# Kernel tuning notes

Measured on AMD Instinct MI355X. Metric: run time of the kernel, lower is better.

The kernel has to match this reference:

```python
import jax, jax.numpy as jnp
import numpy as np
from jax import lax

B, T_ENC, E = 32, 256, 512
A_RNN, D_RNN, P = 1024, 1024, 256
N_MEL, T_DEC = 80, 800
A_DIM, N_FILT, K = 128, 32, 31
PAD = (K - 1) // 2


def setup_inputs() -> dict:
    key = jax.random.key(0)
    ks = jax.random.split(key, 20)
    rn = lambda k, s, sc=0.02: jax.random.normal(k, s, dtype=jnp.float32) * sc
    return {
        "encoder_outputs": jax.random.normal(ks[0], (B, T_ENC, E), dtype=jnp.float32),
        "decoder_inputs": jax.random.normal(ks[1], (B, N_MEL, T_DEC), dtype=jnp.float32),
        "input_lengths": jax.random.randint(ks[2], (B,), 128, T_ENC + 1),
        "prenet_w1": rn(ks[3], (P, N_MEL)),
        "prenet_w2": rn(ks[4], (P, P)),
        "attn_rnn_Wih": rn(ks[5], (4 * A_RNN, P + E)),
        "attn_rnn_Whh": rn(ks[6], (4 * A_RNN, A_RNN)),
        "attn_rnn_bih": jnp.zeros((4 * A_RNN,), jnp.float32),
        "attn_rnn_bhh": jnp.zeros((4 * A_RNN,), jnp.float32),
        "query_W": rn(ks[7], (A_RNN, A_DIM)),
        "memory_W": rn(ks[8], (E, A_DIM)),
        "v_w": rn(ks[9], (A_DIM,)),
        "loc_conv_W": rn(ks[10], (N_FILT, 2, K)),
        "loc_lin_W": rn(ks[11], (N_FILT, A_DIM)),
        "dec_rnn_Wih": rn(ks[12], (4 * D_RNN, A_RNN + E)),
        "dec_rnn_Whh": rn(ks[13], (4 * D_RNN, D_RNN)),
        "dec_rnn_bih": jnp.zeros((4 * D_RNN,), jnp.float32),
        "dec_rnn_bhh": jnp.zeros((4 * D_RNN,), jnp.float32),
        "proj_W": rn(ks[14], (D_RNN + E, N_MEL)),
        "proj_b": jnp.zeros((N_MEL,), jnp.float32),
        "gate_W": rn(ks[15], (D_RNN + E, 1)),
        "gate_b": jnp.zeros((1,), jnp.float32),
    }


def _lstm_cell(xin, h0, c0, Wih, Whh, bih, bhh):
    # PyTorch LSTMCell gate order: i, f, g, o
    g = xin @ Wih.T + bih + h0 @ Whh.T + bhh
    i, f, gg, o = jnp.split(g, 4, axis=-1)
    c = jax.nn.sigmoid(f) * c0 + jax.nn.sigmoid(i) * jnp.tanh(gg)
    return jax.nn.sigmoid(o) * jnp.tanh(c), c


def _forward(encoder_outputs, decoder_inputs, prenet_w1, prenet_w2,
             attn_rnn_Wih, attn_rnn_Whh, attn_rnn_bih, attn_rnn_bhh,
             query_W, memory_W, v_w, loc_conv_W, loc_lin_W,
             dec_rnn_Wih, dec_rnn_Whh, dec_rnn_bih, dec_rnn_bhh,
             proj_W, proj_b, gate_W, gate_b, input_lengths):
    b, t_enc, e = encoder_outputs.shape
    n_mel = decoder_inputs.shape[1]
    dt = encoder_outputs.dtype

    # parse_decoder_inputs + go frame; keep the T_dec frames actually consumed
    x = jnp.transpose(decoder_inputs, (2, 0, 1))               # [T_dec, B, n_mel]
    go = jnp.zeros((1, b, n_mel), dt)
    x = jnp.concatenate([go, x], 0)[:-1]                       # [T_dec, B, n_mel]

    # Prenet: relu->dropout(p=0.5, always on) x2 (deterministic keys)
    k1, k2 = jax.random.split(jax.random.key(42))
    h = jax.nn.relu(jnp.einsum('tbm,pm->tbp', x, prenet_w1))
    h = h * jax.random.bernoulli(k1, 0.5, h.shape) * 2.0
    h = jax.nn.relu(jnp.einsum('tbp,qp->tbq', h, prenet_w2))
    pre = h * jax.random.bernoulli(k2, 0.5, h.shape) * 2.0     # [T_dec, B, P]

    valid = jnp.arange(t_enc)[None, :] < input_lengths[:, None]  # [B, T_enc]
    pmem = jnp.einsum('bte,ea->bta', encoder_outputs, memory_W)  # processed memory

    def step(carry, xstep):
        ah, ac, dh, dc, ctx, aw, awc = carry
        ah, ac = _lstm_cell(jnp.concatenate([xstep, ctx], -1), ah, ac,
                            attn_rnn_Wih, attn_rnn_Whh, attn_rnn_bih, attn_rnn_bhh)
        # location-sensitive attention (LSA)
        loc = jnp.stack([aw, awc], 1)                           # [B, 2, T_enc]
        lf = lax.conv_general_dilated(loc, loc_conv_W, (1,), [(PAD, PAD)],
                                      dimension_numbers=('NCH', 'OIH', 'NCH'))
        lf = jnp.einsum('bft,fa->bta', lf, loc_lin_W)           # [B, T_enc, A_DIM]
        q = ah @ query_W                                        # [B, A_DIM]
        energies = jnp.tanh(q[:, None, :] + lf + pmem) @ v_w    # [B, T_enc]
        energies = jnp.where(valid, energies, jnp.asarray(-1e9, dt))
        aw = jax.nn.softmax(energies, axis=-1)
        awc = awc + aw
        ctx = jnp.einsum('bt,bte->be', aw, encoder_outputs)
        dh, dc = _lstm_cell(jnp.concatenate([ah, ctx], -1), dh, dc,
                            dec_rnn_Wih, dec_rnn_Whh, dec_rnn_bih, dec_rnn_bhh)
        hc = jnp.concatenate([dh, ctx], -1)
        mel = hc @ proj_W + proj_b                              # [B, n_mel]
        gate = (hc @ gate_W + gate_b)[:, 0]                     # [B]
        return (ah, ac, dh, dc, ctx, aw, awc), (mel, gate, aw)

    z = lambda d: jnp.zeros((b, d), dt)
    carry0 = (z(A_RNN), z(A_RNN), z(D_RNN), z(D_RNN), z(e),
              jnp.zeros((b, t_enc), dt), jnp.zeros((b, t_enc), dt))
    _, (mels, gates, aligns) = lax.scan(step, carry0, pre)

    mel_outputs = jnp.transpose(mels, (1, 2, 0))                # [B, n_mel, T_dec]
    gate_outputs = gates.T                                      # [B, T_dec]
    alignments = jnp.transpose(aligns, (1, 0, 2))               # [B, T_dec, T_enc]
    return mel_outputs, gate_outputs, alignments


def reference(encoder_outputs, decoder_inputs, input_lengths, prenet_w1, prenet_w2,
              attn_rnn_Wih, attn_rnn_Whh, attn_rnn_bih, attn_rnn_bhh,
              query_W, memory_W, v_w, loc_conv_W, loc_lin_W,
              dec_rnn_Wih, dec_rnn_Whh, dec_rnn_bih, dec_rnn_bhh,
              proj_W, proj_b, gate_W, gate_b):
    return _forward(encoder_outputs, decoder_inputs, prenet_w1, prenet_w2,
                    attn_rnn_Wih, attn_rnn_Whh, attn_rnn_bih, attn_rnn_bhh,
                    query_W, memory_W, v_w, loc_conv_W, loc_lin_W,
                    dec_rnn_Wih, dec_rnn_Whh, dec_rnn_bih, dec_rnn_bhh,
                    proj_W, proj_b, gate_W, gate_b, input_lengths)
```

## Files before the change

### kernel.cpp

```cpp
#include <hip/hip_runtime.h>
#include <hip/hip_cooperative_groups.h>
#include <cstdint>
#include <cstddef>

constexpr int TDEC   = 800;
constexpr int KCONV  = 31;

constexpr int AH_OFF   = 0;
constexpr int AC_OFF   = 65536;
constexpr int DH_OFF   = 98304;
constexpr int DC_OFF   = 163840;
constexpr int CTX_OFF  = 196608;
constexpr int AW_OFF   = 229376;
constexpr int AWC_OFF  = 237568;
constexpr int BAR_OFF  = 245760;
constexpr int STATE_FLOATS = 253952;
constexpr int PRE_OFF  = 253952;
constexpr int PMEM_OFF = 6807552;
constexpr int W1T_OFF  = 7856128;
constexpr int W2T_OFF  = 7876608;
constexpr int LINT_OFF = 7942144;

typedef __attribute__((ext_vector_type(4))) float f32x4;
typedef __attribute__((ext_vector_type(4))) unsigned int u32x4;

__device__ __forceinline__ void coh_load4(const float* p, f32x4& v) {
  asm volatile("global_load_dwordx4 %0, %1, off sc0 sc1" : "=v"(v) : "v"(p));
}
__device__ __forceinline__ void coh_load1(const float* p, float& v) {
  asm volatile("global_load_dword %0, %1, off sc0 sc1" : "=v"(v) : "v"(p));
}
__device__ __forceinline__ void coh_store1(float* p, float v) {
  asm volatile("global_store_dword %0, %1, off sc0 sc1" :: "v"(p), "v"(v) : "memory");
}
__device__ __forceinline__ void coh_wait() {
  asm volatile("s_waitcnt vmcnt(0)" ::: "memory");
  __builtin_amdgcn_sched_barrier(0);
}

__device__ __forceinline__ void gbar(uint32_t* slots, uint32_t val) {
  asm volatile("s_waitcnt vmcnt(0)" ::: "memory");
  __syncthreads();
  if (threadIdx.x == 0) {
    uint32_t* p = slots + blockIdx.x;
    asm volatile("global_store_dword %0, %1, off sc0 sc1" :: "v"(p), "v"(val) : "memory");
  }
  if (threadIdx.x < 64) {
    const uint32_t* sp = slots + threadIdx.x * 4;
    while (true) {
      u32x4 v4;
      asm volatile("global_load_dwordx4 %0, %1, off sc0 sc1" : "=v"(v4) : "v"(sp) : "memory");
      asm volatile("s_waitcnt vmcnt(0)" ::: "memory");
      if (v4.x >= val && v4.y >= val && v4.z >= val && v4.w >= val) break;
      __builtin_amdgcn_s_sleep(2);
    }
  }
  __syncthreads();
}

__host__ __device__ inline void tf2x32(uint32_t k0, uint32_t k1, uint32_t& x0, uint32_t& x1) {
  const uint32_t ks2 = k0 ^ k1 ^ 0x1BD11BDAu;
  uint32_t y0 = x0 + k0, y1 = x1 + k1;
#define TFR(r) { y0 += y1; y1 = (y1 << (r)) | (y1 >> (32 - (r))); y1 ^= y0; }
  TFR(13) TFR(15) TFR(26) TFR(6)   y0 += k1;  y1 += ks2 + 1u;
  TFR(17) TFR(29) TFR(16) TFR(24)  y0 += ks2; y1 += k0 + 2u;
  TFR(13) TFR(15) TFR(26) TFR(6)   y0 += k0;  y1 += k1 + 3u;
  TFR(17) TFR(29) TFR(16) TFR(24)  y0 += k1;  y1 += ks2 + 4u;
  TFR(13) TFR(15) TFR(26) TFR(6)   y0 += ks2; y1 += k0 + 5u;
#undef TFR
  x0 = y0; x1 = y1;
}

__device__ inline bool tf_keep(uint32_t ka, uint32_t kb, uint32_t i) {
  uint32_t x0 = 0u, x1 = i;
  tf2x32(ka, kb, x0, x1);
  return (((x0 ^ x1) >> 31) == 0u);
}

__device__ inline float sigm(float x) { return 1.f / (1.f + expf(-x)); }

__global__ __launch_bounds__(256) void transpose_k(const float* __restrict__ src,
                                                   float* __restrict__ dst, int R, int C) {
  int i = blockIdx.x * 256 + threadIdx.x;
  if (i < R * C) { int r = i / C, c = i % C; dst[c * R + r] = src[i]; }
}

__global__ __launch_bounds__(256) void prenet1_kernel(const float* __restrict__ decin,
                                                      const float* __restrict__ w1T,
                                                      float* __restrict__ pre,
                                                      uint32_t ka, uint32_t kb) {
  __shared__ float xs[32][81];
  const int t = blockIdx.x, tid = threadIdx.x;
  for (int f = tid; f < 32 * 80; f += 256) {
    int b = f / 80, m = f % 80;
    xs[b][m] = (t == 0) ? 0.f : decin[b * 64000 + m * 800 + (t - 1)];
  }
  __syncthreads();
  const int p = tid;
  float acc[32];
#pragma unroll
  for (int r = 0; r < 32; ++r) acc[r] = 0.f;
  for (int m = 0; m < 80; ++m) {
    float wv = w1T[m * 256 + p];
#pragma unroll
    for (int r = 0; r < 32; ++r) acc[r] += xs[r][m] * wv;
  }
  float* rowbase = pre + (size_t)t * 32 * 256;
#pragma unroll
  for (int r = 0; r < 32; ++r) {
    float v = fmaxf(acc[r], 0.f);
    uint32_t i = (uint32_t)((t * 32 + r) * 256 + p);
    rowbase[r * 256 + p] = tf_keep(ka, kb, i) ? v * 2.f : 0.f;
  }
}

__global__ __launch_bounds__(256) void prenet2_kernel(const float* __restrict__ w2T,
                                                      float* __restrict__ pre,
                                                      uint32_t ka, uint32_t kb) {
  __shared__ float hs[32][257];
  const int t = blockIdx.x, tid = threadIdx.x;
  float* rowbase = pre + (size_t)t * 32 * 256;
  for (int f = tid; f < 32 * 256; f += 256) {
    int b = f >> 8, k = f & 255;
    hs[b][k] = rowbase[b * 256 + k];
  }
  __syncthreads();
  const int p = tid;
  float acc[32];
#pragma unroll
  for (int r = 0; r < 32; ++r) acc[r] = 0.f;
  for (int k = 0; k < 256; ++k) {
    float wv = w2T[k * 256 + p];
#pragma unroll
    for (int r = 0; r < 32; ++r) acc[r] += hs[r][k] * wv;
  }
#pragma unroll
  for (int r = 0; r < 32; ++r) {
    float v = fmaxf(acc[r], 0.f);
    uint32_t i = (uint32_t)((t * 32 + r) * 256 + p);
    rowbase[r * 256 + p] = tf_keep(ka, kb, i) ? v * 2.f : 0.f;
  }
}

__global__ __launch_bounds__(128) void pmem_kernel(const float* __restrict__ enc,
                                                   const float* __restrict__ memW,
                                                   float* __restrict__ pmem) {
  __shared__ float es[8][513];
  const int b = blockIdx.x >> 5, tg = blockIdx.x & 31, t0 = tg * 8;
  const int tid = threadIdx.x;
  for (int f = tid; f < 8 * 512; f += 128) {
    int rr = f >> 9, e = f & 511;
    es[rr][e] = enc[(size_t)(b * 256 + t0 + rr) * 512 + e];
  }
  __syncthreads();
  float acc[8];
#pragma unroll
  for (int r = 0; r < 8; ++r) acc[r] = 0.f;
  const int a = tid;
  for (int e = 0; e < 512; ++e) {
    float wv = memW[e * 128 + a];
#pragma unroll
    for (int r = 0; r < 8; ++r) acc[r] += es[r][e] * wv;
  }
#pragma unroll
  for (int r = 0; r < 8; ++r) pmem[(size_t)(b * 256 + t0 + r) * 128 + a] = acc[r];
}

struct ScanParams {
  const float* enc; const int* lens;
  const float* aWih; const float* aWhh; const float* abih; const float* abhh;
  const float* qW;   const float* vw;   const float* locW; const float* linT;
  const float* dWih; const float* dWhh; const float* dbih; const float* dbhh;
  const float* pW;   const float* pb;   const float* gW;   const float* gb;
  float* ah; float* ac; float* dh; float* dc; float* ctx; float* aw; float* awc;
  uint32_t* bar;
  const float* pre; const float* pmem;
  float* mel_out; float* gate_out; float* align_out;
};

constexpr int SMEM_F = 12480;

struct XW { const float* x; int ldx; const float* w; int ldw; int coh; };

__device__ __forceinline__ void stage_load(const XW& ch, f32x4* sreg, int tid) {
#pragma unroll
  for (int u = 0; u < 2; ++u) {
    int f4 = tid * 2 + u;
    int bs = f4 >> 6;
    int kk = (f4 & 63) * 4;
    const float* p = ch.x + (size_t)bs * ch.ldx + kk;
    if (ch.coh) coh_load4(p, sreg[u]);
    else        sreg[u] = *(const f32x4*)p;
  }
}
__device__ __forceinline__ void stage_store(const f32x4* sreg, float* dst, int tid) {
#pragma unroll
  for (int u = 0; u < 2; ++u) {
    int f4 = tid * 2 + u;
    int bs = f4 >> 6;
    int kk = (f4 & 63) * 4;
    *(f32x4*)(dst + bs * 256 + kk) = sreg[u];
  }
}

template <typename F>
__device__ __forceinline__ void lstm_core(int blk, int tid, int nc, F getc,
                                          const float* bih, const float* bhh,
                                          float* hout, float* cst, float* smem) {
  const int lane = tid & 63;
  const int bg = (tid >> 6) & 3;
  const int jg = tid >> 8;
  const int b0 = bg * 8;
  const int hb = blk * 4;
  float* xs = smem;
  float* gate_s = smem + 8192;

  float acc[4][8];
#pragma unroll
  for (int rr = 0; rr < 4; ++rr) {
    float bv = (lane == 0) ? (bih[jg * 1024 + hb + rr] + bhh[jg * 1024 + hb + rr]) : 0.f;
#pragma unroll
    for (int bb = 0; bb < 8; ++bb) acc[rr][bb] = bv;
  }

  f32x4 sreg[2];
  {
    XW c0 = getc(0);
    stage_load(c0, sreg, tid);
    coh_wait();
    stage_store(sreg, xs, tid);
  }
  float4 wc[4];
  {
    XW c0 = getc(0);
#pragma unroll
    for (int rr = 0; rr < 4; ++rr)
      wc[rr] = *(const float4*)(c0.w + (size_t)(jg * 1024 + hb + rr) * c0.ldw + lane * 4);
  }
  __syncthreads();

  for (int c = 0; c < nc; ++c) {
    float4 wn[4];
    const bool more = (c + 1 < nc);
    if (more) {
      XW cn = getc(c + 1);
      stage_load(cn, sreg, tid);
#pragma unroll
      for (int rr = 0; rr < 4; ++rr)
        wn[rr] = *(const float4*)(cn.w + (size_t)(jg * 1024 + hb + rr) * cn.ldw + lane * 4);
    }
#pragma unroll
    for (int bb = 0; bb < 8; ++bb) {
      float4 x4 = *(const float4*)(xs + (b0 + bb) * 256 + lane * 4);
#pragma unroll
      for (int rr = 0; rr < 4; ++rr) {
        acc[rr][bb] = fmaf(wc[rr].x, x4.x, acc[rr][bb]);
        acc[rr][bb] = fmaf(wc[rr].y, x4.y, acc[rr][bb]);
        acc[rr][bb] = fmaf(wc[rr].z, x4.z, acc[rr][bb]);
        acc[rr][bb] = fmaf(wc[rr].w, x4.w, acc[rr][bb]);
      }
    }
    __syncthreads();
    if (more) {
      coh_wait();
      stage_store(sreg, xs, tid);
#pragma unroll
      for (int rr = 0; rr < 4; ++rr) wc[rr] = wn[rr];
      __syncthreads();
    }
  }

  float v[32];
#pragma unroll
  for (int rr = 0; rr < 4; ++rr)
#pragma unroll
    for (int bb = 0; bb < 8; ++bb) v[rr * 8 + bb] = acc[rr][bb];
#pragma unroll
  for (int s = 0; s < 5; ++s) {
    const int d = 32 >> s;
    const int half = 32 >> (s + 1);
    const bool up = (lane & d) != 0;
#pragma unroll
    for (int i = 0; i < 16; ++i) {
      if (i < half) {
        float send = up ? v[i] : v[i + half];
        float got = __shfl_xor(send, d);
        v[i] = (up ? v[i + half] : v[i]) + got;
      }
    }
  }
  v[0] += __shfl_xor(v[0], 1);
  if ((lane & 1) == 0) {
    int p = (lane >> 1) & 31;
    int rr = p >> 3, bb = p & 7;
    gate_s[(jg * 4 + rr) * 33 + (b0 + bb)] = v[0];
  }
  __syncthreads();
  if (tid < 128) {
    int hl = tid >> 5, b = tid & 31;
    float gi = gate_s[(0 + hl) * 33 + b];
    float gf = gate_s[(4 + hl) * 33 + b];
    float gg = gate_s[(8 + hl) * 33 + b];
    float go = gate_s[(12 + hl) * 33 + b];
    int idx = b * 1024 + hb + hl;
    float c0v = cst[idx];
    float cn = sigm(gf) * c0v + sigm(gi) * tanhf(gg);
    cst[idx] = cn;
    coh_store1(hout + idx, sigm(go) * tanhf(cn));
  }
  __syncthreads();
}

__device__ void stage_attn(int b, int tid, int t, const ScanParams& P,
                           const float* ah_cur, float* ctx_out, float* smem) {
  float* part = smem;
  float* sLoc = smem + 1024;
  float* q_s  = smem + 1600;
  float* vw_s = smem + 1728;
  float* red  = smem + 1856;
  float* aw_s = smem + 1888;
  float* cpart= smem + 2144;
  float* ah_l = smem + 3168;
  float* lf_s = smem + 4192;

  float ahv;
  coh_load1(ah_cur + b * 1024 + tid, ahv);
  if (tid < 572) {
    int c = tid / 286, i = tid % 286;
    int src = i - 15;
    float vv = 0.f;
    if (src >= 0 && src < 256) vv = (c == 0 ? P.aw : P.awc)[b * 256 + src];
    sLoc[c * 286 + i] = vv;
  } else if (tid < 700) {
    vw_s[tid - 572] = P.vw[tid - 572];
  }
  coh_wait();
  ah_l[tid] = ahv;
  __syncthreads();
  {
    const int js = tid >> 7, a = tid & 127;
    const float* ahb = ah_l + js * 128;
    const float* qp = P.qW + (size_t)(js * 128) * 128 + a;
    float p0 = 0.f, p1 = 0.f, p2 = 0.f, p3 = 0.f;
    for (int j = 0; j < 128; j += 4) {
      p0 += ahb[j] * qp[(size_t)j * 128];
      p1 += ahb[j + 1] * qp[(size_t)(j + 1) * 128];
      p2 += ahb[j + 2] * qp[(size_t)(j + 2) * 128];
      p3 += ahb[j + 3] * qp[(size_t)(j + 3) * 128];
    }
    part[tid] = (p0 + p1) + (p2 + p3);
  }
  __syncthreads();
  if (tid < 128) {
    float q = 0.f;
#pragma unroll
    for (int js = 0; js < 8; ++js) q += part[js * 128 + tid];
    q_s[tid] = q;
  }
  {
    const int f = tid >> 5, tg = tid & 31;
    float accL[8];
#pragma unroll
    for (int i = 0; i < 8; ++i) accL[i] = 0.f;
    const float* wf = P.locW + f * 62;
#pragma unroll
    for (int c = 0; c < 2; ++c)
#pragma unroll
      for (int k = 0; k < KCONV; ++k) {
        float wv = wf[c * 31 + k];
        const float* sl = sLoc + c * 286 + tg * 8 + k;
#pragma unroll
        for (int i = 0; i < 8; ++i) accL[i] += sl[i] * wv;
      }
#pragma unroll
    for (int i = 0; i < 8; ++i) lf_s[f * 258 + tg * 8 + i] = accL[i];
  }
  __syncthreads();
  {
    const int tt = tid >> 2, aq = tid & 3;
    float lfv[32];
#pragma unroll
    for (int f = 0; f < 32; ++f) lfv[f] = lf_s[f * 258 + tt];
    const float* pm = P.pmem + (size_t)(b * 256 + tt) * 128;
    float ep = 0.f;
#pragma unroll 4
    for (int ai = 0; ai < 32; ++ai) {
      int a = aq * 32 + ai;
      const float4* lt = (const float4*)(P.linT + a * 32);
      float lfa = 0.f;
#pragma unroll
      for (int u = 0; u < 8; ++u) {
        float4 l4 = lt[u];
        lfa += l4.x * lfv[u * 4] + l4.y * lfv[u * 4 + 1] + l4.z * lfv[u * 4 + 2] + l4.w * lfv[u * 4 + 3];
      }
      float val = tanhf(q_s[a] + lfa + pm[a]);
      ep += val * vw_s[a];
    }
    part[tid] = ep;
  }
  __syncthreads();
  const int len_b = P.lens[b];
  if (tid < 256) {
    float e = part[tid * 4] + part[tid * 4 + 1] + part[tid * 4 + 2] + part[tid * 4 + 3];
    e = (tid < len_b) ? e : -1e9f;
    aw_s[tid] = e;
  }
  __syncthreads();
  if (tid < 64) {
    float m0 = fmaxf(fmaxf(aw_s[tid], aw_s[64 + tid]), fmaxf(aw_s[128 + tid], aw_s[192 + tid]));
#pragma unroll
    for (int m = 32; m >= 1; m >>= 1) m0 = fmaxf(m0, __shfl_xor(m0, m));
    if (tid == 0) red[0] = m0;
  }
  __syncthreads();
  const float mx = red[0];
  if (tid < 256) part[tid] = expf(aw_s[tid] - mx);
  __syncthreads();
  if (tid < 64) {
    float s0 = part[tid] + part[64 + tid] + part[128 + tid] + part[192 + tid];
#pragma unroll
    for (int m = 32; m >= 1; m >>= 1) s0 += __shfl_xor(s0, m);
    if (tid == 0) red[1] = s0;
  }
  __syncthreads();
  const float inv = 1.f / red[1];
  if (tid < 256) {
    float awv = part[tid] * inv;
    aw_s[tid] = awv;
    P.aw[b * 256 + tid] = awv;
    P.awc[b * 256 + tid] += awv;
    P.align_out[(size_t)b * 204800 + (size_t)t * 256 + tid] = awv;
  }
  __syncthreads();
  {
    const int ee = tid & 511, hf = tid >> 9;
    const float* encb = P.enc + (size_t)b * 131072 + (size_t)hf * 128 * 512 + ee;
    float a0 = 0.f, a1 = 0.f, a2 = 0.f, a3 = 0.f;
    for (int tt = 0; tt < 128; tt += 4) {
      a0 += aw_s[hf * 128 + tt] * encb[(size_t)tt * 512];
      a1 += aw_s[hf * 128 + tt + 1] * encb[(size_t)(tt + 1) * 512];
      a2 += aw_s[hf * 128 + tt + 2] * encb[(size_t)(tt + 2) * 512];
      a3 += aw_s[hf * 128 + tt + 3] * encb[(size_t)(tt + 3) * 512];
    }
    cpart[hf * 512 + ee] = (a0 + a1) + (a2 + a3);
  }
  __syncthreads();
  if (tid < 512) coh_store1(ctx_out + b * 512 + tid, cpart[tid] + cpart[512 + tid]);
}

__device__ void stage_proj(int b, int tid, int tp, const ScanParams& P,
                           const float* dh_prev, const float* ctx_prev, float* smem) {
  float* hc    = smem;
  float* partm = smem + 1536;
  float* partg = smem + 2016;
  for (int i = tid; i < 1536; i += 1024) {
    float v;
    const float* p = (i < 1024) ? (dh_prev + b * 1024 + i) : (ctx_prev + b * 512 + (i - 1024));
    coh_load1(p, v);
    coh_wait();
    hc[i] = v;
  }
  __syncthreads();
  if (tid < 480) {
    int ks = tid / 80, m = tid % 80;
    const float* pWk = P.pW + (size_t)(ks * 256) * 80 + m;
    const float* hck = hc + ks * 256;
    float a0 = 0.f, a1 = 0.f, a2 = 0.f, a3 = 0.f;
    for (int k = 0; k < 256; k += 4) {
      a0 += hck[k] * pWk[(size_t)k * 80];
      a1 += hck[k + 1] * pWk[(size_t)(k + 1) * 80];
      a2 += hck[k + 2] * pWk[(size_t)(k + 2) * 80];
      a3 += hck[k + 3] * pWk[(size_t)(k + 3) * 80];
    }
    partm[ks * 80 + m] = (a0 + a1) + (a2 + a3);
  } else if (tid < 512) {
    int s = tid - 480;
    float acc = 0.f;
    for (int k = s * 48; k < s * 48 + 48; ++k) acc += hc[k] * P.gW[k];
    partg[s] = acc;
  }
  __syncthreads();
  if (tid < 80) {
    float acc = P.pb[tid];
#pragma unroll
    for (int s = 0; s < 6; ++s) acc += partm[s * 80 + tid];
    P.mel_out[b * 64000 + tid * 800 + tp] = acc;
  }
  if (tid == 511) {
    float acc = P.gb[0];
#pragma unroll
    for (int s = 0; s < 32; ++s) acc += partg[s];
    P.gate_out[b * 800 + tp] = acc;
  }
  __syncthreads();
}

__global__ void __launch_bounds__(1024, 4) scan_kernel(ScanParams P) {
  const int blk = blockIdx.x, tid = threadIdx.x;
  __shared__ float smem[SMEM_F];
  uint32_t* slots = P.bar;
  uint32_t bk = 0;

  for (int i = 0; i <= TDEC; ++i) {
    const int pi = i & 1, pim1 = pi ^ 1;
    if (i < TDEC) {
      const float* pre_t = P.pre + (size_t)i * 8192;
      const float* ctx_r = P.ctx + pim1 * 16384;
      const float* ah_r  = P.ah + pim1 * 32768;
      const ScanParams& Q = P;
      auto getc1 = [&](int c) -> XW {
        XW r;
        if (c == 0)      { r.x = pre_t;                 r.ldx = 256;  r.w = Q.aWih;                        r.ldw = 768;  r.coh = 0; }
        else if (c <= 2) { r.x = ctx_r + (c - 1) * 256; r.ldx = 512;  r.w = Q.aWih + 256 + (c - 1) * 256;  r.ldw = 768;  r.coh = 1; }
        else             { r.x = ah_r + (c - 3) * 256;  r.ldx = 1024; r.w = Q.aWhh + (c - 3) * 256;        r.ldw = 1024; r.coh = 1; }
        return r;
      };
      lstm_core(blk, tid, 7, getc1, P.abih, P.abhh, P.ah + pi * 32768, P.ac, smem);
    }
    if (i >= 1) {
      const float* ah_r  = P.ah + pim1 * 32768;
      const float* ctx_r = P.ctx + pim1 * 16384;
      const float* dh_r  = P.dh + pi * 32768;
      const ScanParams& Q = P;
      auto getc2 = [&](int c) -> XW {
        XW r;
        if (c <= 3)      { r.x = ah_r + c * 256;        r.ldx = 1024; r.w = Q.dWih + c * 256;              r.ldw = 1536; r.coh = 1; }
        else if (c <= 5) { r.x = ctx_r + (c - 4) * 256; r.ldx = 512;  r.w = Q.dWih + 1024 + (c - 4) * 256; r.ldw = 1536; r.coh = 1; }
        else             { r.x = dh_r + (c - 6) * 256;  r.ldx = 1024; r.w = Q.dWhh + (c - 6) * 256;        r.ldw = 1024; r.coh = 1; }
        return r;
      };
      lstm_core(blk, tid, 10, getc2, P.dbih, P.dbhh, P.dh + pim1 * 32768, P.dc, smem);
    }
    gbar(slots, ++bk);
    if (blk < 32) {
      if (i < TDEC) stage_attn(blk, tid, i, P, P.ah + pi * 32768, P.ctx + pi * 16384, smem);
    } else if (blk < 64) {
      if (i >= 1) stage_proj(blk - 32, tid, i - 1, P, P.dh + pim1 * 32768, P.ctx + pim1 * 16384, smem);
    }
    gbar(slots, ++bk);
  }
}

extern "C" void kernel_launch(void* const* d_in, const int* in_sizes, int n_in,
                              void* d_out, int out_size, void* d_ws, size_t ws_size,
                              hipStream_t stream) {
  (void)in_sizes; (void)n_in; (void)out_size; (void)ws_size;
  const float* enc   = (const float*)d_in[0];
  const float* decin = (const float*)d_in[1];
  const int*   lens  = (const int*)d_in[2];
  const float* w1    = (const float*)d_in[3];
  const float* w2    = (const float*)d_in[4];
  const float* aWih  = (const float*)d_in[5];
  const float* aWhh  = (const float*)d_in[6];
  const float* abih  = (const float*)d_in[7];
  const float* abhh  = (const float*)d_in[8];
  const float* qW    = (const float*)d_in[9];
  const float* memW  = (const float*)d_in[10];
  const float* vw    = (const float*)d_in[11];
  const float* locW  = (const float*)d_in[12];
  const float* linW  = (const float*)d_in[13];
  const float* dWih  = (const float*)d_in[14];
  const float* dWhh  = (const float*)d_in[15];
  const float* dbih  = (const float*)d_in[16];
  const float* dbhh  = (const float*)d_in[17];
  const float* pW    = (const float*)d_in[18];
  const float* pb    = (const float*)d_in[19];
  const float* gW    = (const float*)d_in[20];
  const float* gb    = (const float*)d_in[21];

  float* ws  = (float*)d_ws;
  float* out = (float*)d_out;

  hipMemsetAsync(ws, 0, (size_t)STATE_FLOATS * sizeof(float), stream);

  uint32_t k1a, k1b, k2a, k2b;
  { uint32_t a = 0u, b = 0u; tf2x32(0u, 42u, a, b); k1a = a; k1b = b; }
  { uint32_t a = 0u, b = 1u; tf2x32(0u, 42u, a, b); k2a = a; k2b = b; }

  transpose_k<<<dim3((256 * 80 + 255) / 256), dim3(256), 0, stream>>>(w1, ws + W1T_OFF, 256, 80);
  transpose_k<<<dim3((256 * 256 + 255) / 256), dim3(256), 0, stream>>>(w2, ws + W2T_OFF, 256, 256);
  transpose_k<<<dim3((32 * 128 + 255) / 256), dim3(256), 0, stream>>>(linW, ws + LINT_OFF, 32, 128);
  prenet1_kernel<<<dim3(800), dim3(256), 0, stream>>>(decin, ws + W1T_OFF, ws + PRE_OFF, k1a, k1b);
  prenet2_kernel<<<dim3(800), dim3(256), 0, stream>>>(ws + W2T_OFF, ws + PRE_OFF, k2a, k2b);
  pmem_kernel<<<dim3(1024), dim3(128), 0, stream>>>(enc, memW, ws + PMEM_OFF);

  ScanParams prm;
  prm.enc = enc; prm.lens = lens;
  prm.aWih = aWih; prm.aWhh = aWhh; prm.abih = abih; prm.abhh = abhh;
  prm.qW = qW; prm.vw = vw; prm.locW = locW; prm.linT = ws + LINT_OFF;
  prm.dWih = dWih; prm.dWhh = dWhh; prm.dbih = dbih; prm.dbhh = dbhh;
  prm.pW = pW; prm.pb = pb; prm.gW = gW; prm.gb = gb;
  prm.ah = ws + AH_OFF; prm.ac = ws + AC_OFF;
  prm.dh = ws + DH_OFF; prm.dc = ws + DC_OFF;
  prm.ctx = ws + CTX_OFF; prm.aw = ws + AW_OFF; prm.awc = ws + AWC_OFF;
  prm.bar = (uint32_t*)(ws + BAR_OFF);
  prm.pre = ws + PRE_OFF; prm.pmem = ws + PMEM_OFF;
  prm.mel_out = out; prm.gate_out = out + 2048000; prm.align_out = out + 2073600;

  void* kargs[] = { (void*)&prm };
  hipLaunchCooperativeKernel(scan_kernel, dim3(256), dim3(1024), kargs, 0, stream);
}
```

Before: 382.4 ms.

## Keep LSTM weight high halves resident in LDS and stream low halves from a prepacked blob

Each of the 256 persistent blocks now splits its slice of the attention and decoder LSTM weights into high and low 16-bit halves. The high halves are kept resident in LDS for the whole 800-step scan, and the low halves are read from a prepacked, lane-ordered global blob built by a new pre-kernel. The full fp32 weight is rebuilt in registers, so each step no longer re-reads all fp32 weights from global memory or L2. The location-conv/energy stage is also reorganised into two 128-position halves with a shuffle reduction so it fits the smaller scratch area. This costs about 160KB of dynamic LDS per block, which limits occupancy, and adds a one-time packing pass at kernel start.

Measured after the change: 391.7 ms. 1.02x slower.

```diff
diff --git a/kernel.cpp b/kernel.cpp
--- a/kernel.cpp
+++ b/kernel.cpp
@@ -2,9 +2,9 @@
 #include <hip/hip_cooperative_groups.h>
 #include <cstdint>
 #include <cstddef>
+#include <cstring>
 
 constexpr int TDEC   = 800;
-constexpr int KCONV  = 31;
 
 constexpr int AH_OFF   = 0;
 constexpr int AC_OFF   = 65536;
@@ -20,6 +20,13 @@
 constexpr int W1T_OFF  = 7856128;
 constexpr int W2T_OFF  = 7876608;
 constexpr int LINT_OFF = 7942144;
+constexpr int BLOB_OFF = 7946240;
+constexpr int WCHUNKS_A = 14;
+constexpr int WCHUNKS_D = 20;
+constexpr int WBLK_DW  = 34816;
+
+constexpr int SCRATCH_F     = 5376;
+constexpr int SMEM_BYTES    = 139264 + SCRATCH_F * 4;
 
 typedef __attribute__((ext_vector_type(4))) float f32x4;
 typedef __attribute__((ext_vector_type(4))) unsigned int u32x4;
@@ -79,6 +86,20 @@
 
 __device__ inline float sigm(float x) { return 1.f / (1.f + expf(-x)); }
 
+__device__ __forceinline__ const float* wsrc(int c, int j, int kk,
+                                             const float* aWih, const float* aWhh,
+                                             const float* dWih, const float* dWhh) {
+  if (c < WCHUNKS_A) {
+    int k = c * 128 + kk;
+    return (k < 768) ? (aWih + (size_t)j * 768 + k)
+                     : (aWhh + (size_t)j * 1024 + (k - 768));
+  } else {
+    int k = (c - WCHUNKS_A) * 128 + kk;
+    return (k < 1536) ? (dWih + (size_t)j * 1536 + k)
+                      : (dWhh + (size_t)j * 1024 + (k - 1536));
+  }
+}
+
 __global__ __launch_bounds__(256) void transpose_k(const float* __restrict__ src,
                                                    float* __restrict__ dst, int R, int C) {
   int i = blockIdx.x * 256 + threadIdx.x;
@@ -166,6 +187,29 @@
   for (int r = 0; r < 8; ++r) pmem[(size_t)(b * 256 + t0 + r) * 128 + a] = acc[r];
 }
 
+__global__ __launch_bounds__(1024) void mklo_kernel(const float* __restrict__ aWih,
+                                                    const float* __restrict__ aWhh,
+                                                    const float* __restrict__ dWih,
+                                                    const float* __restrict__ dWhh,
+                                                    uint32_t* __restrict__ blob) {
+  __shared__ float tmp[2048];
+  const int blk = blockIdx.x, tid = threadIdx.x;
+  uint32_t* bdst = blob + (size_t)blk * WBLK_DW;
+  for (int c = 0; c < WCHUNKS_A + WCHUNKS_D; ++c) {
+    const int row16 = tid >> 6;
+    const int kk = (tid & 63) * 2;
+    const int j = (row16 >> 2) * 1024 + blk * 4 + (row16 & 3);
+    float2 wv = *(const float2*)wsrc(c, j, kk, aWih, aWhh, dWih, dWhh);
+    *(float2*)(tmp + row16 * 128 + kk) = wv;
+    __syncthreads();
+    const int rr = tid & 3, jgq = (tid >> 2) & 3, l = tid >> 4;
+    uint32_t b0 = __float_as_uint(tmp[(jgq * 4 + rr) * 128 + l * 2]) & 0xffffu;
+    uint32_t b1 = __float_as_uint(tmp[(jgq * 4 + rr) * 128 + l * 2 + 1]) & 0xffffu;
+    bdst[c * 1024 + (l * 4 + jgq) * 4 + rr] = b0 | (b1 << 16);
+    __syncthreads();
+  }
+}
+
 struct ScanParams {
   const float* enc; const int* lens;
   const float* aWih; const float* aWhh; const float* abih; const float* abhh;
@@ -173,47 +217,25 @@
   const float* dWih; const float* dWhh; const float* dbih; const float* dbhh;
   const float* pW;   const float* pb;   const float* gW;   const float* gb;
   float* ah; float* ac; float* dh; float* dc; float* ctx; float* aw; float* awc;
-  uint32_t* bar;
+  uint32_t* bar; const uint32_t* wlo;
   const float* pre; const float* pmem;
   float* mel_out; float* gate_out; float* align_out;
 };
 
-constexpr int SMEM_F = 12480;
-
-struct XW { const float* x; int ldx; const float* w; int ldw; int coh; };
-
-__device__ __forceinline__ void stage_load(const XW& ch, f32x4* sreg, int tid) {
-#pragma unroll
-  for (int u = 0; u < 2; ++u) {
-    int f4 = tid * 2 + u;
-    int bs = f4 >> 6;
-    int kk = (f4 & 63) * 4;
-    const float* p = ch.x + (size_t)bs * ch.ldx + kk;
-    if (ch.coh) coh_load4(p, sreg[u]);
-    else        sreg[u] = *(const f32x4*)p;
-  }
-}
-__device__ __forceinline__ void stage_store(const f32x4* sreg, float* dst, int tid) {
-#pragma unroll
-  for (int u = 0; u < 2; ++u) {
-    int f4 = tid * 2 + u;
-    int bs = f4 >> 6;
-    int kk = (f4 & 63) * 4;
-    *(f32x4*)(dst + bs * 256 + kk) = sreg[u];
-  }
-}
+struct XW { const float* x; int ldx; int coh; };
 
 template <typename F>
-__device__ __forceinline__ void lstm_core(int blk, int tid, int nc, F getc,
-                                          const float* bih, const float* bhh,
-                                          float* hout, float* cst, float* smem) {
+__device__ __forceinline__ void lstm_lds(int blk, int tid, int nc, F getx,
+                                         const uint32_t* wch0, const uint32_t* lch0,
+                                         const float* bih, const float* bhh,
+                                         float* hout, float* cst,
+                                         float* xs, float* gate_s) {
   const int lane = tid & 63;
   const int bg = (tid >> 6) & 3;
   const int jg = tid >> 8;
   const int b0 = bg * 8;
-  const int hb = blk * 4;
-  float* xs = smem;
-  float* gate_s = smem + 8192;
+  const int hb = blk << 2;
+  const int woff = (lane * 4 + jg) << 2;
 
   float acc[4][8];
 #pragma unroll
@@ -223,49 +245,49 @@
     for (int bb = 0; bb < 8; ++bb) acc[rr][bb] = bv;
   }
 
-  f32x4 sreg[2];
+  const int sb = tid >> 5;
+  const int skq = (tid & 31) * 4;
+  f32x4 sreg;
+  u32x4 lcur, lnxt;
   {
-    XW c0 = getc(0);
-    stage_load(c0, sreg, tid);
-    coh_wait();
-    stage_store(sreg, xs, tid);
-  }
-  float4 wc[4];
-  {
-    XW c0 = getc(0);
-#pragma unroll
-    for (int rr = 0; rr < 4; ++rr)
-      wc[rr] = *(const float4*)(c0.w + (size_t)(jg * 1024 + hb + rr) * c0.ldw + lane * 4);
+    XW x0 = getx(0);
+    const float* p = x0.x + (size_t)sb * x0.ldx + skq;
+    lcur = *(const u32x4*)(lch0 + woff);
+    if (x0.coh) { coh_load4(p, sreg); coh_wait(); }
+    else        sreg = *(const f32x4*)p;
+    *(f32x4*)(xs + sb * 132 + skq) = sreg;
   }
   __syncthreads();
 
   for (int c = 0; c < nc; ++c) {
-    float4 wn[4];
     const bool more = (c + 1 < nc);
     if (more) {
-      XW cn = getc(c + 1);
-      stage_load(cn, sreg, tid);
+      XW xn = getx(c + 1);
+      const float* p = xn.x + (size_t)sb * xn.ldx + skq;
+      lnxt = *(const u32x4*)(lch0 + (c + 1) * 1024 + woff);
+      if (xn.coh) coh_load4(p, sreg);
+      else        sreg = *(const f32x4*)p;
+    }
+    u32x4 wv = *(const u32x4*)(wch0 + c * 1024 + woff);
+    float we[4], wo[4];
+#pragma unroll
+    for (int rr = 0; rr < 4; ++rr) {
+      uint32_t h = wv[rr], l = lcur[rr];
+      we[rr] = __uint_as_float((h << 16) | (l & 0xffffu));
+      wo[rr] = __uint_as_float((h & 0xffff0000u) | (l >> 16));
+    }
+#pragma unroll
+    for (int bb = 0; bb < 8; ++bb) {
+      float2 x2 = *(const float2*)(xs + (b0 + bb) * 132 + lane * 2);
 #pragma unroll
       for (int rr = 0; rr < 4; ++rr)
-        wn[rr] = *(const float4*)(cn.w + (size_t)(jg * 1024 + hb + rr) * cn.ldw + lane * 4);
-    }
-#pragma unroll
-    for (int bb = 0; bb < 8; ++bb) {
-      float4 x4 = *(const float4*)(xs + (b0 + bb) * 256 + lane * 4);
-#pragma unroll
-      for (int rr = 0; rr < 4; ++rr) {
-        acc[rr][bb] = fmaf(wc[rr].x, x4.x, acc[rr][bb]);
-        acc[rr][bb] = fmaf(wc[rr].y, x4.y, acc[rr][bb]);
-        acc[rr][bb] = fmaf(wc[rr].z, x4.z, acc[rr][bb]);
-        acc[rr][bb] = fmaf(wc[rr].w, x4.w, acc[rr][bb]);
-      }
+        acc[rr][bb] = fmaf(wo[rr], x2.y, fmaf(we[rr], x2.x, acc[rr][bb]));
     }
     __syncthreads();
     if (more) {
       coh_wait();
-      stage_store(sreg, xs, tid);
-#pragma unroll
-      for (int rr = 0; rr < 4; ++rr) wc[rr] = wn[rr];
+      *(f32x4*)(xs + sb * 132 + skq) = sreg;
+      lcur = lnxt;
       __syncthreads();
     }
   }
@@ -312,16 +334,16 @@
 }
 
 __device__ void stage_attn(int b, int tid, int t, const ScanParams& P,
-                           const float* ah_cur, float* ctx_out, float* smem) {
-  float* part = smem;
-  float* sLoc = smem + 1024;
-  float* q_s  = smem + 1600;
-  float* vw_s = smem + 1728;
-  float* red  = smem + 1856;
-  float* aw_s = smem + 1888;
-  float* cpart= smem + 2144;
-  float* ah_l = smem + 3168;
-  float* lf_s = smem + 4192;
+                           const float* ah_cur, float* ctx_out, float* S) {
+  float* ah_l = S;
+  float* part = S + 1024;
+  float* lf   = S;
+  float* sLoc = S + 4224;
+  float* q_s  = S + 4800;
+  float* vw_s = S + 4928;
+  float* red  = S + 5056;
+  float* aw_s = S + 5064;
+  float* cpart= S + 1024;
 
   float ahv;
   coh_load1(ah_cur + b * 1024 + tid, ahv);
@@ -357,55 +379,54 @@
     for (int js = 0; js < 8; ++js) q += part[js * 128 + tid];
     q_s[tid] = q;
   }
-  {
-    const int f = tid >> 5, tg = tid & 31;
-    float accL[8];
-#pragma unroll
-    for (int i = 0; i < 8; ++i) accL[i] = 0.f;
-    const float* wf = P.locW + f * 62;
-#pragma unroll
-    for (int c = 0; c < 2; ++c)
-#pragma unroll
-      for (int k = 0; k < KCONV; ++k) {
-        float wv = wf[c * 31 + k];
-        const float* sl = sLoc + c * 286 + tg * 8 + k;
-#pragma unroll
-        for (int i = 0; i < 8; ++i) accL[i] += sl[i] * wv;
+  __syncthreads();
+  const int len_b = P.lens[b];
+#pragma unroll 1
+  for (int h = 0; h < 2; ++h) {
+    const int tt0 = h << 7;
+    {
+      const int f = tid >> 5, seg = tid & 31;
+      float a0 = 0.f, a1 = 0.f, a2 = 0.f, a3 = 0.f;
+      const float* wf = P.locW + f * 62;
+#pragma unroll
+      for (int c2 = 0; c2 < 2; ++c2)
+#pragma unroll
+        for (int k = 0; k < 31; ++k) {
+          float wv = wf[c2 * 31 + k];
+          const float* sl = sLoc + c2 * 286 + tt0 + seg * 4 + k;
+          a0 = fmaf(sl[0], wv, a0); a1 = fmaf(sl[1], wv, a1);
+          a2 = fmaf(sl[2], wv, a2); a3 = fmaf(sl[3], wv, a3);
+        }
+      lf[(seg * 4 + 0) * 33 + f] = a0; lf[(seg * 4 + 1) * 33 + f] = a1;
+      lf[(seg * 4 + 2) * 33 + f] = a2; lf[(seg * 4 + 3) * 33 + f] = a3;
+    }
+    __syncthreads();
+    {
+      const int ttl = tid >> 3, aq = tid & 7;
+      const int tt = tt0 + ttl;
+      const float* pm = P.pmem + (size_t)(b * 256 + tt) * 128;
+      const float* lfr = lf + ttl * 33;
+      float lfv[32];
+#pragma unroll
+      for (int f = 0; f < 32; ++f) lfv[f] = lfr[f];
+      float ep = 0.f;
+#pragma unroll 2
+      for (int ai = 0; ai < 16; ++ai) {
+        int a = aq * 16 + ai;
+        const float4* lt = (const float4*)(P.linT + a * 32);
+        float lfa = 0.f;
+#pragma unroll
+        for (int u = 0; u < 8; ++u) {
+          float4 l4 = lt[u];
+          lfa += l4.x * lfv[u * 4] + l4.y * lfv[u * 4 + 1] + l4.z * lfv[u * 4 + 2] + l4.w * lfv[u * 4 + 3];
+        }
+        ep += vw_s[a] * tanhf(q_s[a] + lfa + pm[a]);
       }
-#pragma unroll
-    for (int i = 0; i < 8; ++i) lf_s[f * 258 + tg * 8 + i] = accL[i];
-  }
-  __syncthreads();
-  {
-    const int tt = tid >> 2, aq = tid & 3;
-    float lfv[32];
-#pragma unroll
-    for (int f = 0; f < 32; ++f) lfv[f] = lf_s[f * 258 + tt];
-    const float* pm = P.pmem + (size_t)(b * 256 + tt) * 128;
-    float ep = 0.f;
-#pragma unroll 4
-    for (int ai = 0; ai < 32; ++ai) {
-      int a = aq * 32 + ai;
-      const float4* lt = (const float4*)(P.linT + a * 32);
-      float lfa = 0.f;
-#pragma unroll
-      for (int u = 0; u < 8; ++u) {
-        float4 l4 = lt[u];
-        lfa += l4.x * lfv[u * 4] + l4.y * lfv[u * 4 + 1] + l4.z * lfv[u * 4 + 2] + l4.w * lfv[u * 4 + 3];
-      }
-      float val = tanhf(q_s[a] + lfa + pm[a]);
-      ep += val * vw_s[a];
-    }
-    part[tid] = ep;
-  }
-  __syncthreads();
-  const int len_b = P.lens[b];
-  if (tid < 256) {
-    float e = part[tid * 4] + part[tid * 4 + 1] + part[tid * 4 + 2] + part[tid * 4 + 3];
-    e = (tid < len_b) ? e : -1e9f;
-    aw_s[tid] = e;
-  }
-  __syncthreads();
+      ep += __shfl_xor(ep, 1); ep += __shfl_xor(ep, 2); ep += __shfl_xor(ep, 4);
+      if (aq == 0) aw_s[tt] = (tt < len_b) ? ep : -1e9f;
+    }
+    __syncthreads();
+  }
   if (tid < 64) {
     float m0 = fmaxf(fmaxf(aw_s[tid], aw_s[64 + tid]), fmaxf(aw_s[128 + tid], aw_s[192 + tid]));
 #pragma unroll
@@ -414,10 +435,10 @@
   }
   __syncthreads();
   const float mx = red[0];
-  if (tid < 256) part[tid] = expf(aw_s[tid] - mx);
+  if (tid < 256) aw_s[tid] = expf(aw_s[tid] - mx);
   __syncthreads();
   if (tid < 64) {
-    float s0 = part[tid] + part[64 + tid] + part[128 + tid] + part[192 + tid];
+    float s0 = aw_s[tid] + aw_s[64 + tid] + aw_s[128 + tid] + aw_s[192 + tid];
 #pragma unroll
     for (int m = 32; m >= 1; m >>= 1) s0 += __shfl_xor(s0, m);
     if (tid == 0) red[1] = s0;
@@ -425,7 +446,7 @@
   __syncthreads();
   const float inv = 1.f / red[1];
   if (tid < 256) {
-    float awv = part[tid] * inv;
+    float awv = aw_s[tid] * inv;
     aw_s[tid] = awv;
     P.aw[b * 256 + tid] = awv;
     P.awc[b * 256 + tid] += awv;
@@ -449,10 +470,10 @@
 }
 
 __device__ void stage_proj(int b, int tid, int tp, const ScanParams& P,
-                           const float* dh_prev, const float* ctx_prev, float* smem) {
-  float* hc    = smem;
-  float* partm = smem + 1536;
-  float* partg = smem + 2016;
+                           const float* dh_prev, const float* ctx_prev, float* S) {
+  float* hc    = S;
+  float* partm = S + 1536;
+  float* partg = S + 2016;
   for (int i = tid; i < 1536; i += 1024) {
     float v;
     const float* p = (i < 1024) ? (dh_prev + b * 1024 + i) : (ctx_prev + b * 512 + (i - 1024));
@@ -496,8 +517,32 @@
 }
 
 __global__ void __launch_bounds__(1024, 4) scan_kernel(ScanParams P) {
+  extern __shared__ char dynsmem[];
+  uint32_t* wlds = (uint32_t*)dynsmem;
+  float* scratch = (float*)(dynsmem + 139264);
+  float* xs = scratch;
+  float* gate_s = scratch + 4224;
   const int blk = blockIdx.x, tid = threadIdx.x;
-  __shared__ float smem[SMEM_F];
+
+  {
+    float* tmp = xs;
+    for (int c = 0; c < WCHUNKS_A + WCHUNKS_D; ++c) {
+      const int row16 = tid >> 6;
+      const int kk = (tid & 63) * 2;
+      const int j = (row16 >> 2) * 1024 + blk * 4 + (row16 & 3);
+      float2 wv = *(const float2*)wsrc(c, j, kk, P.aWih, P.aWhh, P.dWih, P.dWhh);
+      *(float2*)(tmp + row16 * 128 + kk) = wv;
+      __syncthreads();
+      const int rr = tid & 3, jgq = (tid >> 2) & 3, l = tid >> 4;
+      uint32_t hi0 = __float_as_uint(tmp[(jgq * 4 + rr) * 128 + l * 2]) >> 16;
+      uint32_t hi1 = __float_as_uint(tmp[(jgq * 4 + rr) * 128 + l * 2 + 1]) >> 16;
+      wlds[c * 1024 + (l * 4 + jgq) * 4 + rr] = hi0 | (hi1 << 16);
+      __syncthreads();
+    }
+  }
+  __syncthreads();
+
+  const uint32_t* lblk = P.wlo + (size_t)blk * WBLK_DW;
   uint32_t* slots = P.bar;
   uint32_t bk = 0;
 
@@ -507,35 +552,36 @@
       const float* pre_t = P.pre + (size_t)i * 8192;
       const float* ctx_r = P.ctx + pim1 * 16384;
       const float* ah_r  = P.ah + pim1 * 32768;
-      const ScanParams& Q = P;
-      auto getc1 = [&](int c) -> XW {
+      auto getxA = [&](int c) -> XW {
         XW r;
-        if (c == 0)      { r.x = pre_t;                 r.ldx = 256;  r.w = Q.aWih;                        r.ldw = 768;  r.coh = 0; }
-        else if (c <= 2) { r.x = ctx_r + (c - 1) * 256; r.ldx = 512;  r.w = Q.aWih + 256 + (c - 1) * 256;  r.ldw = 768;  r.coh = 1; }
-        else             { r.x = ah_r + (c - 3) * 256;  r.ldx = 1024; r.w = Q.aWhh + (c - 3) * 256;        r.ldw = 1024; r.coh = 1; }
+        if (c < 2)      { r.x = pre_t + c * 128;        r.ldx = 256;  r.coh = 0; }
+        else if (c < 6) { r.x = ctx_r + (c - 2) * 128;  r.ldx = 512;  r.coh = 1; }
+        else            { r.x = ah_r + (c - 6) * 128;   r.ldx = 1024; r.coh = 1; }
         return r;
       };
-      lstm_core(blk, tid, 7, getc1, P.abih, P.abhh, P.ah + pi * 32768, P.ac, smem);
+      lstm_lds(blk, tid, WCHUNKS_A, getxA, wlds, lblk, P.abih, P.abhh,
+               P.ah + pi * 32768, P.ac, xs, gate_s);
     }
     if (i >= 1) {
-      const float* ah_r  = P.ah + pim1 * 32768;
-      const float* ctx_r = P.ctx + pim1 * 16384;
+      const float* ah_w  = P.ah + pim1 * 32768;
+      const float* ctx_w = P.ctx + pim1 * 16384;
       const float* dh_r  = P.dh + pi * 32768;
-      const ScanParams& Q = P;
-      auto getc2 = [&](int c) -> XW {
+      auto getxD = [&](int c) -> XW {
         XW r;
-        if (c <= 3)      { r.x = ah_r + c * 256;        r.ldx = 1024; r.w = Q.dWih + c * 256;              r.ldw = 1536; r.coh = 1; }
-        else if (c <= 5) { r.x = ctx_r + (c - 4) * 256; r.ldx = 512;  r.w = Q.dWih + 1024 + (c - 4) * 256; r.ldw = 1536; r.coh = 1; }
-        else             { r.x = dh_r + (c - 6) * 256;  r.ldx = 1024; r.w = Q.dWhh + (c - 6) * 256;        r.ldw = 1024; r.coh = 1; }
+        if (c < 8)       { r.x = ah_w + c * 128;         r.ldx = 1024; r.coh = 1; }
+        else if (c < 12) { r.x = ctx_w + (c - 8) * 128;  r.ldx = 512;  r.coh = 1; }
+        else             { r.x = dh_r + (c - 12) * 128;  r.ldx = 1024; r.coh = 1; }
         return r;
       };
-      lstm_core(blk, tid, 10, getc2, P.dbih, P.dbhh, P.dh + pim1 * 32768, P.dc, smem);
+      lstm_lds(blk, tid, WCHUNKS_D, getxD, wlds + WCHUNKS_A * 1024,
+               lblk + WCHUNKS_A * 1024, P.dbih, P.dbhh,
+               P.dh + pim1 * 32768, P.dc, xs, gate_s);
     }
     gbar(slots, ++bk);
     if (blk < 32) {
-      if (i < TDEC) stage_attn(blk, tid, i, P, P.ah + pi * 32768, P.ctx + pi * 16384, smem);
+      if (i < TDEC) stage_attn(blk, tid, i, P, P.ah + pi * 32768, P.ctx + pi * 16384, scratch);
     } else if (blk < 64) {
-      if (i >= 1) stage_proj(blk - 32, tid, i - 1, P, P.dh + pim1 * 32768, P.ctx + pim1 * 16384, smem);
+      if (i >= 1) stage_proj(blk - 32, tid, i - 1, P, P.dh + pim1 * 32768, P.ctx + pim1 * 16384, scratch);
     }
     gbar(slots, ++bk);
   }
@@ -571,7 +617,7 @@
   float* ws  = (float*)d_ws;
   float* out = (float*)d_out;
 
-  hipMemsetAsync(ws, 0, (size_t)STATE_FLOATS * sizeof(float), stream);
+  (void)hipMemsetAsync(ws, 0, (size_t)STATE_FLOATS * sizeof(float), stream);
 
   uint32_t k1a, k1b, k2a, k2b;
   { uint32_t a = 0u, b = 0u; tf2x32(0u, 42u, a, b); k1a = a; k1b = b; }
@@ -583,6 +629,8 @@
   prenet1_kernel<<<dim3(800), dim3(256), 0, stream>>>(decin, ws + W1T_OFF, ws + PRE_OFF, k1a, k1b);
   prenet2_kernel<<<dim3(800), dim3(256), 0, stream>>>(ws + W2T_OFF, ws + PRE_OFF, k2a, k2b);
   pmem_kernel<<<dim3(1024), dim3(128), 0, stream>>>(enc, memW, ws + PMEM_OFF);
+  mklo_kernel<<<dim3(256), dim3(1024), 0, stream>>>(aWih, aWhh, dWih, dWhh,
+                                                    (uint32_t*)(ws + BLOB_OFF));
 
   ScanParams prm;
   prm.enc = enc; prm.lens = lens;
@@ -594,9 +642,13 @@
   prm.dh = ws + DH_OFF; prm.dc = ws + DC_OFF;
   prm.ctx = ws + CTX_OFF; prm.aw = ws + AW_OFF; prm.awc = ws + AWC_OFF;
   prm.bar = (uint32_t*)(ws + BAR_OFF);
+  prm.wlo = (const uint32_t*)(ws + BLOB_OFF);
   prm.pre = ws + PRE_OFF; prm.pmem = ws + PMEM_OFF;
   prm.mel_out = out; prm.gate_out = out + 2048000; prm.align_out = out + 2073600;
 
+  (void)hipFuncSetAttribute((const void*)scan_kernel,
+                            hipFuncAttributeMaxDynamicSharedMemorySize, SMEM_BYTES);
+
   void* kargs[] = { (void*)&prm };
-  hipLaunchCooperativeKernel(scan_kernel, dim3(256), dim3(1024), kargs, 0, stream);
-}
+  (void)hipLaunchCooperativeKernel(scan_kernel, dim3(256), dim3(1024), kargs, SMEM_BYTES, stream);
+}
```
